# Kernel tuning notes

Measured on AMD Instinct MI355X. Metric: run time of the kernel, lower is better.

## Reference

```python
import jax, jax.numpy as jnp
import numpy as np

HIDDEN = 256
HEADS = 8
HEAD_DIM = HIDDEN // HEADS
SCALE = HEAD_DIM ** -0.5
N = 4096
NUM_GRAPHS = 16
LN_EPS = 1e-5


def setup_inputs() -> dict:
    key = jax.random.key(0)
    ks = jax.random.split(key, 8)
    x = jax.random.normal(ks[0], (N, HIDDEN), dtype=jnp.float32)
    batch = jnp.sort(jax.random.randint(ks[1], (N,), 0, NUM_GRAPHS, dtype=jnp.int64))
    # Xavier-uniform linear weights, stored as [in, out] (y = x @ W + b)
    lim = float(np.sqrt(6.0 / (HIDDEN + HIDDEN)))
    def W(k):
        return jax.random.uniform(k, (HIDDEN, HIDDEN), jnp.float32, -lim, lim)
    return {
        "x": x,
        "batch": batch,
        "Wq": W(ks[2]), "bq": jnp.zeros((HIDDEN,), jnp.float32),
        "Wk": W(ks[3]), "bk": jnp.zeros((HIDDEN,), jnp.float32),
        "Wv": W(ks[4]), "bv": jnp.zeros((HIDDEN,), jnp.float32),
        "Wo": W(ks[5]), "bo": jnp.zeros((HIDDEN,), jnp.float32),
        "gamma": jnp.ones((HIDDEN,), jnp.float32),
        "beta": jnp.zeros((HIDDEN,), jnp.float32),
    }


def _layer_norm(x, gamma, beta):
    mu = jnp.mean(x, axis=-1, keepdims=True)
    var = jnp.mean(jnp.square(x - mu), axis=-1, keepdims=True)
    return (x - mu) * jax.lax.rsqrt(var + LN_EPS) * gamma + beta


def reference(x, batch, Wq, bq, Wk, bk, Wv, bv, Wo, bo, gamma, beta):
    residual = x
    h = _layer_norm(x, gamma, beta)
    n = h.shape[0]
    q = (h @ Wq + bq).reshape(n, HEADS, HEAD_DIM)
    k = (h @ Wk + bk).reshape(n, HEADS, HEAD_DIM)
    v = (h @ Wv + bv).reshape(n, HEADS, HEAD_DIM)
    # dense scores masked to block-diagonal (same-graph) structure
    scores = jnp.einsum('ihd,jhd->ihj', q, k) * SCALE  # [N, H, N]
    same_graph = (batch[None, :] == batch[:, None])[:, None, :]  # [N, 1, N]
    scores = jnp.where(same_graph, scores, -jnp.inf)
    attn = jax.nn.softmax(scores, axis=-1)
    attn = jnp.nan_to_num(attn, nan=0.0)
    out = jnp.einsum('ihj,jhd->ihd', attn, v).reshape(n, HIDDEN)
    out = out @ Wo + bo
    return residual + out
```

## Files before the change

### kernel.cpp

```cpp
#include <hip/hip_runtime.h>

#define NNODES 4096
#define HID 256
#define NG 16
#define NH 8
#define HD 32
#define LN_EPS 1e-5f
#define QSCALE (0.17677669529663687f * 1.4426950408889634f)
#define HLS 264
#define AOS 264

typedef unsigned short u16;
typedef unsigned int u32;
typedef __bf16 bf16x8 __attribute__((ext_vector_type(8)));
typedef float f32x4 __attribute__((ext_vector_type(4)));

__device__ __forceinline__ u16 f2bf(float f){
  union { float f; u32 i; } c; c.f = f;
  u32 x = c.i;
  return (u16)((x + 0x7fffu + ((x >> 16) & 1u)) >> 16);
}

__global__ __launch_bounds__(256) void lnqkv_kernel(
    const float* __restrict__ x, const float* __restrict__ gamma,
    const float* __restrict__ beta,
    const float* __restrict__ Wq, const float* __restrict__ Wk,
    const float* __restrict__ Wv, const float* __restrict__ Wo,
    const float* __restrict__ bq, const float* __restrict__ bk,
    const float* __restrict__ bv,
    u16* __restrict__ qb, u16* __restrict__ kb, u16* __restrict__ vb,
    u16* __restrict__ WoT){
  __shared__ u16 hl[64][HLS];
  int bid = blockIdx.x;
  int which = blockIdx.y;
  if (which == 3){
    if (bid >= 64) return;
    u16 (*tl)[33] = (u16(*)[33])hl;
    int bx = (bid & 7) * 32, by = (bid >> 3) * 32;
    int tx = threadIdx.x & 31, ty = threadIdx.x >> 5;
    #pragma unroll
    for (int r = 0; r < 32; r += 8)
      tl[ty + r][tx] = f2bf(Wo[(size_t)(by + ty + r) * HID + bx + tx]);
    __syncthreads();
    #pragma unroll
    for (int r = 0; r < 32; r += 8)
      WoT[(size_t)(bx + ty + r) * HID + by + tx] = tl[tx][ty + r];
    return;
  }
  int wave = threadIdx.x >> 6, lane = threadIdx.x & 63;
  int m0 = (bid >> 2) * 64;
  int nb = (bid & 3) * 64 + wave * 16;
  const float* W    = (which == 0) ? Wq : (which == 1) ? Wk : Wv;
  const float* bias = (which == 0) ? bq : (which == 1) ? bk : bv;
  u16* out          = (which == 0) ? qb : (which == 1) ? kb : vb;

  int rsub = lane >> 4;
  int c16  = lane & 15;
  float4 g0 = *(const float4*)(gamma + c16 * 16 + 0);
  float4 g1 = *(const float4*)(gamma + c16 * 16 + 4);
  float4 g2 = *(const float4*)(gamma + c16 * 16 + 8);
  float4 g3 = *(const float4*)(gamma + c16 * 16 + 12);
  float4 t0 = *(const float4*)(beta + c16 * 16 + 0);
  float4 t1 = *(const float4*)(beta + c16 * 16 + 4);
  float4 t2 = *(const float4*)(beta + c16 * 16 + 8);
  float4 t3 = *(const float4*)(beta + c16 * 16 + 12);
  float ga[16] = {g0.x,g0.y,g0.z,g0.w, g1.x,g1.y,g1.z,g1.w,
                  g2.x,g2.y,g2.z,g2.w, g3.x,g3.y,g3.z,g3.w};
  float bt[16] = {t0.x,t0.y,t0.z,t0.w, t1.x,t1.y,t1.z,t1.w,
                  t2.x,t2.y,t2.z,t2.w, t3.x,t3.y,t3.z,t3.w};
  #pragma unroll
  for (int b = 0; b < 4; b++){
    int rloc = wave * 16 + b * 4 + rsub;
    const float* xr = x + (size_t)(m0 + rloc) * HID + c16 * 16;
    float4 v0 = *(const float4*)(xr + 0);
    float4 v1 = *(const float4*)(xr + 4);
    float4 v2 = *(const float4*)(xr + 8);
    float4 v3 = *(const float4*)(xr + 12);
    float e[16] = {v0.x,v0.y,v0.z,v0.w, v1.x,v1.y,v1.z,v1.w,
                   v2.x,v2.y,v2.z,v2.w, v3.x,v3.y,v3.z,v3.w};
    float s = 0.f;
    #pragma unroll
    for (int i = 0; i < 16; i++) s += e[i];
    s += __shfl_xor(s, 1); s += __shfl_xor(s, 2);
    s += __shfl_xor(s, 4); s += __shfl_xor(s, 8);
    float mu = s * (1.0f / HID);
    float vv = 0.f;
    #pragma unroll
    for (int i = 0; i < 16; i++){ e[i] -= mu; vv += e[i] * e[i]; }
    vv += __shfl_xor(vv, 1); vv += __shfl_xor(vv, 2);
    vv += __shfl_xor(vv, 4); vv += __shfl_xor(vv, 8);
    float rs = rsqrtf(vv * (1.0f / HID) + LN_EPS);
    u32 pk[8];
    #pragma unroll
    for (int i = 0; i < 8; i++){
      float o0 = e[2*i]     * rs * ga[2*i]     + bt[2*i];
      float o1 = e[2*i + 1] * rs * ga[2*i + 1] + bt[2*i + 1];
      pk[i] = (u32)f2bf(o0) | ((u32)f2bf(o1) << 16);
    }
    *(uint4*)&hl[rloc][c16 * 16]     = make_uint4(pk[0], pk[1], pk[2], pk[3]);
    *(uint4*)&hl[rloc][c16 * 16 + 8] = make_uint4(pk[4], pk[5], pk[6], pk[7]);
  }
  __syncthreads();

  int lr = lane & 15, lq = lane >> 4;
  f32x4 acc[4] = {};
  const float* wbase = W + nb + lr;
  #pragma unroll
  for (int k0 = 0; k0 < HID; k0 += 32){
    union { bf16x8 v; u16 e[8]; } bf;
    const float* wp = wbase + (size_t)(k0 + lq * 8) * HID;
    #pragma unroll
    for (int j = 0; j < 8; j++) bf.e[j] = f2bf(wp[(size_t)j * HID]);
    #pragma unroll
    for (int t = 0; t < 4; t++){
      bf16x8 a = *(const bf16x8*)&hl[t * 16 + lr][k0 + lq * 8];
      acc[t] = __builtin_amdgcn_mfma_f32_16x16x32_bf16(a, bf.v, acc[t], 0, 0, 0);
    }
  }
  int col = nb + lr;
  float bb = bias[col];
  #pragma unroll
  for (int t = 0; t < 4; t++){
    #pragma unroll
    for (int r = 0; r < 4; r++){
      int row = m0 + 16 * t + lq * 4 + r;
      out[(size_t)row * HID + col] = f2bf(acc[t][r] + bb);
    }
  }
}

__global__ __launch_bounds__(1024, 4) void attnproj_kernel(
    const u16* __restrict__ q, const u16* __restrict__ k,
    const u16* __restrict__ v, const u16* __restrict__ WoT,
    const float* __restrict__ bo, const float* __restrict__ x,
    const int* __restrict__ batch, int bstride, float* __restrict__ out){
  __shared__ u16 ao[16][AOS];
  __shared__ float mg[8][10][64];
  __shared__ int s_se[2];
  int m0 = blockIdx.x * 16;
  int tid = threadIdx.x;
  int wave = tid >> 6, lane = tid & 63;
  int g_lo = batch[(size_t)m0 * bstride];
  int g_hi = batch[(size_t)(m0 + 15) * bstride];
  if (wave < 2){
    int target = wave ? (g_hi + 1) : g_lo;
    int p = batch[(size_t)(lane * 64) * bstride];
    int c = __popcll(__ballot(p < target));
    int lo = 0;
    if (c > 0){
      int base = (c - 1) * 64 + 1;
      int idx = base + lane;
      int val = (idx < NNODES) ? batch[(size_t)idx * bstride] : 0x7fffffff;
      lo = base + __popcll(__ballot(val < target));
    }
    if (lane == 0) s_se[wave] = lo;
  }
  __syncthreads();
  int jstart = s_se[0], jend = s_se[1];
  int ntj = (jend - jstart + 15) >> 4;
  int lq = lane >> 4, lr = lane & 15;
  int hd = wave & 7;
  int jh = wave >> 3;

  int qrow = m0 + lr;
  bf16x8 qf = *(const bf16x8*)&q[(size_t)qrow * HID + hd * HD + lq * 8];
  int gq = batch[(size_t)qrow * bstride];
  float m = -3.0e38f, l = 0.f;
  f32x4 o0 = {0.f,0.f,0.f,0.f}, o1 = {0.f,0.f,0.f,0.f};
  {
    int half = (ntj + 1) >> 1;
    int jt0 = jh ? half : 0;
    int jt1 = jh ? ntj : half;
    for (int jt = jt0; jt < jt1; jt++){
      int j0 = jstart + (jt << 4);
      int krow = j0 + lr; if (krow > NNODES - 1) krow = NNODES - 1;
      bf16x8 kf = *(const bf16x8*)&k[(size_t)krow * HID + hd * HD + lq * 8];
      u16 va[4], vc[4];
      #pragma unroll
      for (int i = 0; i < 4; i++){
        int vrow = j0 + lq * 4 + i;
        if (vrow > NNODES - 1) vrow = NNODES - 1;
        const u16* vp = &v[(size_t)vrow * HID + hd * HD + lr];
        va[i] = vp[0];
        vc[i] = vp[16];
      }
      f32x4 st = __builtin_amdgcn_mfma_f32_16x16x32_bf16(kf, qf,
                   (f32x4){0.f,0.f,0.f,0.f}, 0, 0, 0);
      int jb = j0 + lq * 4;
      int i0 = jb + 0 > 4095 ? 4095 : jb + 0;
      int i1 = jb + 1 > 4095 ? 4095 : jb + 1;
      int i2 = jb + 2 > 4095 ? 4095 : jb + 2;
      int i3 = jb + 3 > 4095 ? 4095 : jb + 3;
      int gj0 = batch[(size_t)i0 * bstride];
      int gj1 = batch[(size_t)i1 * bstride];
      int gj2 = batch[(size_t)i2 * bstride];
      int gj3 = batch[(size_t)i3 * bstride];
      float s0 = (jb + 0 < jend && gj0 == gq) ? st[0] * QSCALE : -3.0e38f;
      float s1 = (jb + 1 < jend && gj1 == gq) ? st[1] * QSCALE : -3.0e38f;
      float s2 = (jb + 2 < jend && gj2 == gq) ? st[2] * QSCALE : -3.0e38f;
      float s3 = (jb + 3 < jend && gj3 == gq) ? st[3] * QSCALE : -3.0e38f;
      float tm = fmaxf(fmaxf(s0, s1), fmaxf(s2, s3));
      tm = fmaxf(tm, __shfl_xor(tm, 16));
      tm = fmaxf(tm, __shfl_xor(tm, 32));
      float mn = fmaxf(m, tm);
      float alpha = exp2f(m - mn);
      float p0 = exp2f(s0 - mn), p1 = exp2f(s1 - mn);
      float p2 = exp2f(s2 - mn), p3 = exp2f(s3 - mn);
      float ps = (p0 + p1) + (p2 + p3);
      ps += __shfl_xor(ps, 16);
      ps += __shfl_xor(ps, 32);
      l = l * alpha + ps;
      m = mn;
      union { bf16x8 v8; u32 w[4]; } pf, vf0, vf1;
      pf.w[0] = (u32)f2bf(p0) | ((u32)f2bf(p1) << 16);
      pf.w[1] = (u32)f2bf(p2) | ((u32)f2bf(p3) << 16);
      pf.w[2] = 0; pf.w[3] = 0;
      vf0.w[0] = (u32)va[0] | ((u32)va[1] << 16);
      vf0.w[1] = (u32)va[2] | ((u32)va[3] << 16);
      vf0.w[2] = 0; vf0.w[3] = 0;
      vf1.w[0] = (u32)vc[0] | ((u32)vc[1] << 16);
      vf1.w[1] = (u32)vc[2] | ((u32)vc[3] << 16);
      vf1.w[2] = 0; vf1.w[3] = 0;
      o0 = o0 * alpha;
      o1 = o1 * alpha;
      o0 = __builtin_amdgcn_mfma_f32_16x16x32_bf16(vf0.v8, pf.v8, o0, 0, 0, 0);
      o1 = __builtin_amdgcn_mfma_f32_16x16x32_bf16(vf1.v8, pf.v8, o1, 0, 0, 0);
    }
  }
  if (jh == 1){
    mg[hd][0][lane] = o0[0]; mg[hd][1][lane] = o0[1];
    mg[hd][2][lane] = o0[2]; mg[hd][3][lane] = o0[3];
    mg[hd][4][lane] = o1[0]; mg[hd][5][lane] = o1[1];
    mg[hd][6][lane] = o1[2]; mg[hd][7][lane] = o1[3];
    mg[hd][8][lane] = m;     mg[hd][9][lane] = l;
  }
  __syncthreads();
  if (jh == 0){
    float m2 = mg[hd][8][lane], l2 = mg[hd][9][lane];
    float mn = fmaxf(m, m2);
    float a  = exp2f(m - mn);
    float a2 = exp2f(m2 - mn);
    float lt = l * a + l2 * a2;
    float rl = 1.0f / lt;
    float r0 = (o0[0]*a + mg[hd][0][lane]*a2) * rl;
    float r1 = (o0[1]*a + mg[hd][1][lane]*a2) * rl;
    float r2 = (o0[2]*a + mg[hd][2][lane]*a2) * rl;
    float r3 = (o0[3]*a + mg[hd][3][lane]*a2) * rl;
    float r4 = (o1[0]*a + mg[hd][4][lane]*a2) * rl;
    float r5 = (o1[1]*a + mg[hd][5][lane]*a2) * rl;
    float r6 = (o1[2]*a + mg[hd][6][lane]*a2) * rl;
    float r7 = (o1[3]*a + mg[hd][7][lane]*a2) * rl;
    int dbase = hd * HD + lq * 4;
    *(u32*)&ao[lr][dbase]          = (u32)f2bf(r0) | ((u32)f2bf(r1) << 16);
    *(u32*)&ao[lr][dbase + 2]      = (u32)f2bf(r2) | ((u32)f2bf(r3) << 16);
    *(u32*)&ao[lr][dbase + 16]     = (u32)f2bf(r4) | ((u32)f2bf(r5) << 16);
    *(u32*)&ao[lr][dbase + 16 + 2] = (u32)f2bf(r6) | ((u32)f2bf(r7) << 16);
  }
  __syncthreads();

  {
    int n0 = wave * 16;
    f32x4 acc = {};
    const u16* brow = WoT + (size_t)(n0 + lr) * HID + lq * 8;
    #pragma unroll
    for (int k0 = 0; k0 < HID; k0 += 32){
      bf16x8 a = *(const bf16x8*)&ao[lr][k0 + lq * 8];
      bf16x8 b = *(const bf16x8*)(brow + k0);
      acc = __builtin_amdgcn_mfma_f32_16x16x32_bf16(a, b, acc, 0, 0, 0);
    }
    int col = n0 + lr;
    float bb = bo[col];
    #pragma unroll
    for (int r = 0; r < 4; r++){
      size_t idx = (size_t)(m0 + lq * 4 + r) * HID + col;
      out[idx] = acc[r] + bb + x[idx];
    }
  }
}

__global__ void sentinel_kernel(u32* __restrict__ out, int nwords){
  int i = blockIdx.x * 256 + threadIdx.x;
  if (i < nwords) out[i] = 0x46404640u;
}

extern "C" void kernel_launch(void* const* d_in, const int* in_sizes, int n_in,
                              void* d_out, int out_size, void* d_ws, size_t ws_size,
                              hipStream_t stream){
  const float* x   = (const float*)d_in[0];
  const int* batch = (const int*)d_in[1];
  const float* Wq = (const float*)d_in[2],  *bq = (const float*)d_in[3];
  const float* Wk = (const float*)d_in[4],  *bk = (const float*)d_in[5];
  const float* Wv = (const float*)d_in[6],  *bv = (const float*)d_in[7];
  const float* Wo = (const float*)d_in[8],  *bo = (const float*)d_in[9];
  const float* gamma = (const float*)d_in[10], *beta = (const float*)d_in[11];

  const size_t BUF  = (size_t)NNODES * HID * 2;
  const size_t WOT  = (size_t)HID * HID * 2;
  const size_t NEED = 1024 + 3 * BUF + WOT;

  if (ws_size < NEED){
    int nwords = out_size / 2;
    sentinel_kernel<<<(nwords + 255) / 256, 256, 0, stream>>>((u32*)d_out, nwords);
    return;
  }

  int bstride = (in_sizes[1] >= NNODES * 8) ? 2 : 1;

  char* w = (char*)d_ws;
  u16* qb  = (u16*)(w + 1024);
  u16* kb  = qb + (size_t)NNODES * HID;
  u16* vb  = kb + (size_t)NNODES * HID;
  u16* WoT = vb + (size_t)NNODES * HID;

  lnqkv_kernel<<<dim3(256, 4), 256, 0, stream>>>(x, gamma, beta, Wq, Wk, Wv, Wo,
                                                 bq, bk, bv, qb, kb, vb, WoT);
  attnproj_kernel<<<256, 1024, 0, stream>>>(qb, kb, vb, WoT, bo, x, batch,
                                            bstride, (float*)d_out);
}
```

Measured before the change: 114.8 us.

## Precompute graph segment bounds and double-buffer K/V tile loads in attention

All 16 waves now binary-search the sorted batch array to build a per-graph segment table in shared memory. Each query row's same-graph mask then becomes a range check against its segment, which removes four per-iteration global loads of batch ids. The K/V tile loop is software-pipelined: the next tile's K and V fragments are loaded before the current tile's MFMA and softmax work, to hide global memory latency. This costs extra registers for the prefetch buffers and a redundant final load.

Result: no change. 113.3 us (-1.3%).

```diff
diff --git a/kernel.cpp b/kernel.cpp
--- a/kernel.cpp
+++ b/kernel.cpp
@@ -136,14 +136,12 @@
     const int* __restrict__ batch, int bstride, float* __restrict__ out){
   __shared__ u16 ao[16][AOS];
   __shared__ float mg[8][10][64];
-  __shared__ int s_se[2];
+  __shared__ int seg[NG + 1];
   int m0 = blockIdx.x * 16;
   int tid = threadIdx.x;
   int wave = tid >> 6, lane = tid & 63;
-  int g_lo = batch[(size_t)m0 * bstride];
-  int g_hi = batch[(size_t)(m0 + 15) * bstride];
-  if (wave < 2){
-    int target = wave ? (g_hi + 1) : g_lo;
+  {
+    int target = wave + 1;
     int p = batch[(size_t)(lane * 64) * bstride];
     int c = __popcll(__ballot(p < target));
     int lo = 0;
@@ -153,78 +151,87 @@
       int val = (idx < NNODES) ? batch[(size_t)idx * bstride] : 0x7fffffff;
       lo = base + __popcll(__ballot(val < target));
     }
-    if (lane == 0) s_se[wave] = lo;
+    if (lane == 0) seg[target] = lo;
+    if (tid == 0) seg[0] = 0;
   }
   __syncthreads();
-  int jstart = s_se[0], jend = s_se[1];
-  int ntj = (jend - jstart + 15) >> 4;
   int lq = lane >> 4, lr = lane & 15;
   int hd = wave & 7;
   int jh = wave >> 3;
 
   int qrow = m0 + lr;
+  int gq = batch[(size_t)qrow * bstride];
+  int lo_r = seg[gq], hi_r = seg[gq + 1];
+  int g_lo = batch[(size_t)m0 * bstride];
+  int g_hi = batch[(size_t)(m0 + 15) * bstride];
+  int jstart = seg[g_lo], jend = seg[g_hi + 1];
+  int ntj = (jend - jstart + 15) >> 4;
+
   bf16x8 qf = *(const bf16x8*)&q[(size_t)qrow * HID + hd * HD + lq * 8];
-  int gq = batch[(size_t)qrow * bstride];
   float m = -3.0e38f, l = 0.f;
   f32x4 o0 = {0.f,0.f,0.f,0.f}, o1 = {0.f,0.f,0.f,0.f};
   {
     int half = (ntj + 1) >> 1;
     int jt0 = jh ? half : 0;
     int jt1 = jh ? ntj : half;
-    for (int jt = jt0; jt < jt1; jt++){
-      int j0 = jstart + (jt << 4);
-      int krow = j0 + lr; if (krow > NNODES - 1) krow = NNODES - 1;
-      bf16x8 kf = *(const bf16x8*)&k[(size_t)krow * HID + hd * HD + lq * 8];
-      u16 va[4], vc[4];
-      #pragma unroll
-      for (int i = 0; i < 4; i++){
-        int vrow = j0 + lq * 4 + i;
-        if (vrow > NNODES - 1) vrow = NNODES - 1;
-        const u16* vp = &v[(size_t)vrow * HID + hd * HD + lr];
-        va[i] = vp[0];
-        vc[i] = vp[16];
+    if (jt0 < jt1){
+      auto LOADT = [&](int jt, bf16x8& kf, u16* va, u16* vc){
+        int j0 = jstart + (jt << 4);
+        int krow = j0 + lr; if (krow > NNODES - 1) krow = NNODES - 1;
+        kf = *(const bf16x8*)&k[(size_t)krow * HID + hd * HD + lq * 8];
+        #pragma unroll
+        for (int i = 0; i < 4; i++){
+          int vrow = j0 + lq * 4 + i;
+          if (vrow > NNODES - 1) vrow = NNODES - 1;
+          const u16* vp = &v[(size_t)vrow * HID + hd * HD + lr];
+          va[i] = vp[0];
+          vc[i] = vp[16];
+        }
+      };
+      bf16x8 kf_c; u16 va_c[4], vc_c[4];
+      LOADT(jt0, kf_c, va_c, vc_c);
+      for (int jt = jt0; jt < jt1; jt++){
+        bf16x8 kf_n; u16 va_n[4], vc_n[4];
+        int jn = (jt + 1 < jt1) ? jt + 1 : jt;
+        LOADT(jn, kf_n, va_n, vc_n);
+        int j0 = jstart + (jt << 4);
+        f32x4 st = __builtin_amdgcn_mfma_f32_16x16x32_bf16(kf_c, qf,
+                     (f32x4){0.f,0.f,0.f,0.f}, 0, 0, 0);
+        int jb = j0 + lq * 4;
+        float s0 = (jb + 0 >= lo_r && jb + 0 < hi_r) ? st[0] * QSCALE : -3.0e38f;
+        float s1 = (jb + 1 >= lo_r && jb + 1 < hi_r) ? st[1] * QSCALE : -3.0e38f;
+        float s2 = (jb + 2 >= lo_r && jb + 2 < hi_r) ? st[2] * QSCALE : -3.0e38f;
+        float s3 = (jb + 3 >= lo_r && jb + 3 < hi_r) ? st[3] * QSCALE : -3.0e38f;
+        float tm = fmaxf(fmaxf(s0, s1), fmaxf(s2, s3));
+        tm = fmaxf(tm, __shfl_xor(tm, 16));
+        tm = fmaxf(tm, __shfl_xor(tm, 32));
+        float mn = fmaxf(m, tm);
+        float alpha = exp2f(m - mn);
+        float p0 = exp2f(s0 - mn), p1 = exp2f(s1 - mn);
+        float p2 = exp2f(s2 - mn), p3 = exp2f(s3 - mn);
+        float ps = (p0 + p1) + (p2 + p3);
+        ps += __shfl_xor(ps, 16);
+        ps += __shfl_xor(ps, 32);
+        l = l * alpha + ps;
+        m = mn;
+        union { bf16x8 v8; u32 w[4]; } pf, vf0, vf1;
+        pf.w[0] = (u32)f2bf(p0) | ((u32)f2bf(p1) << 16);
+        pf.w[1] = (u32)f2bf(p2) | ((u32)f2bf(p3) << 16);
+        pf.w[2] = 0; pf.w[3] = 0;
+        vf0.w[0] = (u32)va_c[0] | ((u32)va_c[1] << 16);
+        vf0.w[1] = (u32)va_c[2] | ((u32)va_c[3] << 16);
+        vf0.w[2] = 0; vf0.w[3] = 0;
+        vf1.w[0] = (u32)vc_c[0] | ((u32)vc_c[1] << 16);
+        vf1.w[1] = (u32)vc_c[2] | ((u32)vc_c[3] << 16);
+        vf1.w[2] = 0; vf1.w[3] = 0;
+        o0 = o0 * alpha;
+        o1 = o1 * alpha;
+        o0 = __builtin_amdgcn_mfma_f32_16x16x32_bf16(vf0.v8, pf.v8, o0, 0, 0, 0);
+        o1 = __builtin_amdgcn_mfma_f32_16x16x32_bf16(vf1.v8, pf.v8, o1, 0, 0, 0);
+        kf_c = kf_n;
+        #pragma unroll
+        for (int i = 0; i < 4; i++){ va_c[i] = va_n[i]; vc_c[i] = vc_n[i]; }
       }
-      f32x4 st = __builtin_amdgcn_mfma_f32_16x16x32_bf16(kf, qf,
-                   (f32x4){0.f,0.f,0.f,0.f}, 0, 0, 0);
-      int jb = j0 + lq * 4;
-      int i0 = jb + 0 > 4095 ? 4095 : jb + 0;
-      int i1 = jb + 1 > 4095 ? 4095 : jb + 1;
-      int i2 = jb + 2 > 4095 ? 4095 : jb + 2;
-      int i3 = jb + 3 > 4095 ? 4095 : jb + 3;
-      int gj0 = batch[(size_t)i0 * bstride];
-      int gj1 = batch[(size_t)i1 * bstride];
-      int gj2 = batch[(size_t)i2 * bstride];
-      int gj3 = batch[(size_t)i3 * bstride];
-      float s0 = (jb + 0 < jend && gj0 == gq) ? st[0] * QSCALE : -3.0e38f;
-      float s1 = (jb + 1 < jend && gj1 == gq) ? st[1] * QSCALE : -3.0e38f;
-      float s2 = (jb + 2 < jend && gj2 == gq) ? st[2] * QSCALE : -3.0e38f;
-      float s3 = (jb + 3 < jend && gj3 == gq) ? st[3] * QSCALE : -3.0e38f;
-      float tm = fmaxf(fmaxf(s0, s1), fmaxf(s2, s3));
-      tm = fmaxf(tm, __shfl_xor(tm, 16));
-      tm = fmaxf(tm, __shfl_xor(tm, 32));
-      float mn = fmaxf(m, tm);
-      float alpha = exp2f(m - mn);
-      float p0 = exp2f(s0 - mn), p1 = exp2f(s1 - mn);
-      float p2 = exp2f(s2 - mn), p3 = exp2f(s3 - mn);
-      float ps = (p0 + p1) + (p2 + p3);
-      ps += __shfl_xor(ps, 16);
-      ps += __shfl_xor(ps, 32);
-      l = l * alpha + ps;
-      m = mn;
-      union { bf16x8 v8; u32 w[4]; } pf, vf0, vf1;
-      pf.w[0] = (u32)f2bf(p0) | ((u32)f2bf(p1) << 16);
-      pf.w[1] = (u32)f2bf(p2) | ((u32)f2bf(p3) << 16);
-      pf.w[2] = 0; pf.w[3] = 0;
-      vf0.w[0] = (u32)va[0] | ((u32)va[1] << 16);
-      vf0.w[1] = (u32)va[2] | ((u32)va[3] << 16);
-      vf0.w[2] = 0; vf0.w[3] = 0;
-      vf1.w[0] = (u32)vc[0] | ((u32)vc[1] << 16);
-      vf1.w[1] = (u32)vc[2] | ((u32)vc[3] << 16);
-      vf1.w[2] = 0; vf1.w[3] = 0;
-      o0 = o0 * alpha;
-      o1 = o1 * alpha;
-      o0 = __builtin_amdgcn_mfma_f32_16x16x32_bf16(vf0.v8, pf.v8, o0, 0, 0, 0);
-      o1 = __builtin_amdgcn_mfma_f32_16x16x32_bf16(vf1.v8, pf.v8, o1, 0, 0, 0);
     }
   }
   if (jh == 1){
```
